# Kernel optimization log

Measured on AMD Instinct MI355X. Metric: run time of the kernel, lower is better.

Reference implementation:

```python
import jax, jax.numpy as jnp
import numpy as np

N_NODES = 100_000
N_EDGES = 800_000
D_EDGE = 64
D_NODE = 64
D_GLOBAL = 64
D_IN = D_EDGE + 2 * D_NODE + D_GLOBAL  # 256
D_HID = 128
D_OUT = 64


def setup_inputs() -> dict:
    key = jax.random.key(0)
    ks = jax.random.split(key, 8)
    edge_feats = jax.random.normal(ks[0], (N_EDGES, D_EDGE), dtype=jnp.float32)
    node_feats = jax.random.normal(ks[1], (N_NODES, D_NODE), dtype=jnp.float32)
    global_attr = jax.random.normal(ks[2], (D_GLOBAL,), dtype=jnp.float32)
    senders = jax.random.randint(ks[3], (N_EDGES,), 0, N_NODES, dtype=jnp.int32)
    receivers = jax.random.randint(ks[4], (N_EDGES,), 0, N_NODES, dtype=jnp.int32)
    W1 = jax.random.normal(ks[5], (D_IN, D_HID), dtype=jnp.float32) * (1.0 / np.sqrt(D_IN))
    b1 = jnp.zeros((D_HID,), dtype=jnp.float32)
    W2 = jax.random.normal(ks[6], (D_HID, D_OUT), dtype=jnp.float32) * (1.0 / np.sqrt(D_HID))
    b2 = jnp.zeros((D_OUT,), dtype=jnp.float32)
    return {
        "edge_feats": edge_feats,
        "node_feats": node_feats,
        "global_attr": global_attr,
        "senders": senders,
        "receivers": receivers,
        "W1": W1, "b1": b1, "W2": W2, "b2": b2,
    }


def reference(edge_feats, node_feats, global_attr, senders, receivers, W1, b1, W2, b2):
    # Per-edge concat of [edge.data, receiver.data, sender.data, global.data]
    # (torch.cat order in the original), stacked over all edges.
    E = edge_feats.shape[0]
    recv = node_feats[receivers]          # [E, D_NODE] gather
    send = node_feats[senders]            # [E, D_NODE] gather
    g = jnp.broadcast_to(global_attr[None, :], (E, global_attr.shape[0]))
    x = jnp.concatenate([edge_feats, recv, send, g], axis=-1)  # [E, 256]
    # Updater MLP on the stacked edge batch.
    h = jax.nn.relu(x @ W1 + b1)          # [E, 128]
    out = h @ W2 + b2                     # [E, 64]
    return out
```

## Files before the change

### kernel.cpp

```cpp
#include <hip/hip_runtime.h>
#include <hip/hip_bf16.h>


typedef __bf16 bf16x8 __attribute__((ext_vector_type(8)));
typedef __bf16 bf16x2 __attribute__((ext_vector_type(2)));
typedef float f32x4 __attribute__((ext_vector_type(4)));

#define GRID_MAIN 2048
#define SWZ(x) ((x) ^ (((x) >> 3) & 7))
#define WS_NODEBF_OFF 66560

__global__ void prep_kernel(const float* __restrict__ W1, const float* __restrict__ b1,
                            const float* __restrict__ W2, const float* __restrict__ gattr,
                            __bf16* __restrict__ W1F, __bf16* __restrict__ W2F,
                            float* __restrict__ g1) {
    int tid = blockIdx.x * blockDim.x + threadIdx.x;
    if (tid < 128 * 192) {
        int n = tid / 192, k = tid % 192;
        int w = n >> 5, nt2 = (n >> 4) & 1, c = n & 15;
        int f = k >> 5, g = (k >> 3) & 3, j = k & 7;
        W1F[((((w * 2 + nt2) * 6 + f) * 64) + c + 16 * g) * 8 + j] = (__bf16)W1[k * 128 + n];
    } else if (tid < 128 * 192 + 64 * 128) {
        int t = tid - 128 * 192;
        int n = t / 128, p = t % 128;
        int w = n >> 4, c = n & 15;
        int ks = p >> 5, g = (p >> 3) & 3, j = p & 7;
        int klog = (p >> 5) * 32 + (p & 1) * 16 + ((p >> 1) & 15);
        W2F[(((w * 4 + ks) * 64) + c + 16 * g) * 8 + j] = (__bf16)W2[klog * 64 + n];
    } else if (tid < 128 * 192 + 64 * 128 + 128) {
        int n = tid - (128 * 192 + 64 * 128);
        float acc = b1[n];
        for (int j = 0; j < 64; ++j) acc += gattr[j] * W1[(192 + j) * 128 + n];
        g1[n] = acc;
    }
}

__global__ __launch_bounds__(256) void node_conv_kernel(const float* __restrict__ nf,
                                                        __bf16* __restrict__ nb, int n8) {
    int t = blockIdx.x * blockDim.x + threadIdx.x;
    if (t < n8) {
        f32x4 a = *(const f32x4*)(nf + (long)t * 8);
        f32x4 b = *(const f32x4*)(nf + (long)t * 8 + 4);
        bf16x8 o;
#pragma unroll
        for (int j = 0; j < 4; ++j) { o[j] = (__bf16)a[j]; o[4 + j] = (__bf16)b[j]; }
        *(bf16x8*)(nb + (long)t * 8) = o;
    }
}

__device__ __forceinline__ f32x4 mk4(float v) {
    f32x4 r; r[0] = v; r[1] = v; r[2] = v; r[3] = v; return r;
}

__device__ __forceinline__ bf16x8 cvt8(f32x4 lo, f32x4 hi) {
    bf16x8 t;
#pragma unroll
    for (int j = 0; j < 4; ++j) { t[j] = (__bf16)lo[j]; t[4 + j] = (__bf16)hi[j]; }
    return t;
}

__global__ __launch_bounds__(256) void edge_mlp_kernel(
    const float* __restrict__ edge_feats, const __bf16* __restrict__ node_bf,
    const int* __restrict__ senders, const int* __restrict__ receivers,
    const __bf16* __restrict__ W1F, const __bf16* __restrict__ W2F,
    const float* __restrict__ g1, const float* __restrict__ b2,
    float* __restrict__ out, int E, int numTiles)
{
    __shared__ __bf16 smem[20480];

    const int lane = threadIdx.x & 63;
    const int w    = threadIdx.x >> 6;
    const int c    = lane & 15;
    const int g    = lane >> 4;
    const int G    = gridDim.x;

    bf16x8 wb1[2][6];
#pragma unroll
    for (int nt2 = 0; nt2 < 2; ++nt2)
#pragma unroll
        for (int f = 0; f < 6; ++f)
            wb1[nt2][f] = *(const bf16x8*)(W1F + (((w * 2 + nt2) * 6 + f) * 64 + lane) * 8);
    bf16x8 wb2[4];
#pragma unroll
    for (int ks = 0; ks < 4; ++ks)
        wb2[ks] = *(const bf16x8*)(W2F + ((w * 4 + ks) * 64 + lane) * 8);
    const float g1v0 = g1[w * 32 + c];
    const float g1v1 = g1[w * 32 + 16 + c];
    const float b2v  = b2[w * 16 + c];

    const int sr = SWZ(c * 4 + g);

    auto rowof = [&](int i) {
        long r_ = ((long)blockIdx.x + (long)i * G) * 64 + w * 16 + c;
        return r_ > (long)E - 1 ? (long)E - 1 : r_;
    };

    bf16x8 snr0, snr1, sns0, sns1;
    f32x4 se0, se1, se2, se3;
    int iRa, iSa, iRb, iSb;
    {
        long r0 = rowof(0);
        int iR0 = receivers[r0], iS0 = senders[r0];
        const __bf16* pr = node_bf + ((long)iR0 << 6) + g * 8;
        const __bf16* ps = node_bf + ((long)iS0 << 6) + g * 8;
        snr0 = *(const bf16x8*)(pr);
        snr1 = *(const bf16x8*)(pr + 32);
        sns0 = *(const bf16x8*)(ps);
        sns1 = *(const bf16x8*)(ps + 32);
        const float* pe = edge_feats + (r0 << 6) + g * 8;
        se0 = *(const f32x4*)(pe);      se1 = *(const f32x4*)(pe + 4);
        se2 = *(const f32x4*)(pe + 32); se3 = *(const f32x4*)(pe + 36);
        long r1 = rowof(1);
        iRa = receivers[r1]; iSa = senders[r1];
        long r2 = rowof(2);
        iRb = receivers[r2]; iSb = senders[r2];
    }

    for (int t = blockIdx.x; t < numTiles; t += G) {
        __bf16* ab = smem + w * 3072 + lane * 8;
        *(bf16x8*)(ab)        = cvt8(se0, se1);
        *(bf16x8*)(ab + 512)  = cvt8(se2, se3);
        *(bf16x8*)(ab + 1024) = snr0;
        *(bf16x8*)(ab + 1536) = snr1;
        *(bf16x8*)(ab + 2048) = sns0;
        *(bf16x8*)(ab + 2560) = sns1;

        {
            const __bf16* pr = node_bf + ((long)iRa << 6) + g * 8;
            const __bf16* ps = node_bf + ((long)iSa << 6) + g * 8;
            snr0 = *(const bf16x8*)(pr);
            snr1 = *(const bf16x8*)(pr + 32);
            sns0 = *(const bf16x8*)(ps);
            sns1 = *(const bf16x8*)(ps + 32);
            long rce = rowof(1);
            rce = ((long)t + G) * 64 + w * 16 + c;
            if (rce > (long)E - 1) rce = (long)E - 1;
            const float* pe = edge_feats + (rce << 6) + g * 8;
            se0 = *(const f32x4*)(pe);      se1 = *(const f32x4*)(pe + 4);
            se2 = *(const f32x4*)(pe + 32); se3 = *(const f32x4*)(pe + 36);
            iRa = iRb; iSa = iSb;
            long r3 = ((long)t + 3L * G) * 64 + w * 16 + c;
            if (r3 > (long)E - 1) r3 = (long)E - 1;
            iRb = receivers[r3]; iSb = senders[r3];
        }
        __builtin_amdgcn_sched_barrier(0);

        asm volatile("s_waitcnt lgkmcnt(0)" ::: "memory");
        __builtin_amdgcn_s_barrier();

        f32x4 acc0[4], acc1[4];
#pragma unroll
        for (int mt = 0; mt < 4; ++mt) { acc0[mt] = mk4(g1v0); acc1[mt] = mk4(g1v1); }
#pragma unroll
        for (int mt = 0; mt < 4; ++mt)
#pragma unroll
            for (int f = 0; f < 6; ++f) {
                bf16x8 a = *(const bf16x8*)(smem + ((mt * 6 + f) * 64 + lane) * 8);
                acc0[mt] = __builtin_amdgcn_mfma_f32_16x16x32_bf16(a, wb1[0][f], acc0[mt], 0, 0, 0);
                acc1[mt] = __builtin_amdgcn_mfma_f32_16x16x32_bf16(a, wb1[1][f], acc1[mt], 0, 0, 0);
            }

#pragma unroll
        for (int mt = 0; mt < 4; ++mt)
#pragma unroll
            for (int r = 0; r < 4; ++r) {
                float v0 = acc0[mt][r]; v0 = v0 > 0.f ? v0 : 0.f;
                float v1 = acc1[mt][r]; v1 = v1 > 0.f ? v1 : 0.f;
                bf16x2 pk; pk[0] = (__bf16)v0; pk[1] = (__bf16)v1;
                int s = g * 16 + r * 4 + (c >> 2);
                s = SWZ(s);
                *(bf16x2*)&smem[12288 + (mt * 4 + w) * 512 + s * 8 + ((c & 3) << 1)] = pk;
            }

        asm volatile("s_waitcnt lgkmcnt(0)" ::: "memory");
        __builtin_amdgcn_s_barrier();

        f32x4 acc2[4];
#pragma unroll
        for (int mt = 0; mt < 4; ++mt) acc2[mt] = mk4(b2v);
#pragma unroll
        for (int mt = 0; mt < 4; ++mt)
#pragma unroll
            for (int ks = 0; ks < 4; ++ks) {
                bf16x8 ah = *(const bf16x8*)&smem[12288 + (mt * 4 + ks) * 512 + sr * 8];
                acc2[mt] = __builtin_amdgcn_mfma_f32_16x16x32_bf16(ah, wb2[ks], acc2[mt], 0, 0, 0);
            }

#pragma unroll
        for (int mt = 0; mt < 4; ++mt)
#pragma unroll
            for (int r = 0; r < 4; ++r) {
                long orow = (long)t * 64 + mt * 16 + g * 4 + r;
                if (orow < E) out[orow * 64 + w * 16 + c] = acc2[mt][r];
            }
    }
}

__global__ __launch_bounds__(256) void edge_mlp_fallback(
    const float* __restrict__ edge_feats, const float* __restrict__ node_feats,
    const int* __restrict__ senders, const int* __restrict__ receivers,
    const __bf16* __restrict__ W1F, const __bf16* __restrict__ W2F,
    const float* __restrict__ g1, const float* __restrict__ b2,
    float* __restrict__ out, int E, int numTiles)
{
    __shared__ __bf16 A_lds[4 * 6 * 64 * 8];
    __shared__ __bf16 h_frag[4 * 4 * 64 * 8];
    const int lane = threadIdx.x & 63;
    const int w = threadIdx.x >> 6;
    const int c = lane & 15;
    const int g = lane >> 4;
    const int G = gridDim.x;

    bf16x8 wb1[2][6];
#pragma unroll
    for (int nt2 = 0; nt2 < 2; ++nt2)
#pragma unroll
        for (int f = 0; f < 6; ++f)
            wb1[nt2][f] = *(const bf16x8*)(W1F + (((w * 2 + nt2) * 6 + f) * 64 + lane) * 8);
    bf16x8 wb2[4];
#pragma unroll
    for (int ks = 0; ks < 4; ++ks)
        wb2[ks] = *(const bf16x8*)(W2F + ((w * 4 + ks) * 64 + lane) * 8);
    const float g1v0 = g1[w * 32 + c];
    const float g1v1 = g1[w * 32 + 16 + c];
    const float b2v  = b2[w * 16 + c];

    for (int t = blockIdx.x; t < numTiles; t += G) {
        long rowc = (long)t * 64 + w * 16 + c;
        if (rowc > (long)E - 1) rowc = (long)E - 1;
        int iR = receivers[rowc], iS = senders[rowc];
        const float* pr = node_feats + ((long)iR << 6) + g * 8;
        const float* ps = node_feats + ((long)iS << 6) + g * 8;
        const float* pe = edge_feats + (rowc << 6) + g * 8;
        f32x4 e0a = *(const f32x4*)(pe),      e0b = *(const f32x4*)(pe + 4);
        f32x4 e1a = *(const f32x4*)(pe + 32), e1b = *(const f32x4*)(pe + 36);
        f32x4 r0a = *(const f32x4*)(pr),      r0b = *(const f32x4*)(pr + 4);
        f32x4 r1a = *(const f32x4*)(pr + 32), r1b = *(const f32x4*)(pr + 36);
        f32x4 s0a = *(const f32x4*)(ps),      s0b = *(const f32x4*)(ps + 4);
        f32x4 s1a = *(const f32x4*)(ps + 32), s1b = *(const f32x4*)(ps + 36);

        __bf16* ab = A_lds + w * 6 * 512 + lane * 8;
        *(bf16x8*)(ab)        = cvt8(e0a, e0b);
        *(bf16x8*)(ab + 512)  = cvt8(e1a, e1b);
        *(bf16x8*)(ab + 1024) = cvt8(r0a, r0b);
        *(bf16x8*)(ab + 1536) = cvt8(r1a, r1b);
        *(bf16x8*)(ab + 2048) = cvt8(s0a, s0b);
        *(bf16x8*)(ab + 2560) = cvt8(s1a, s1b);
        __syncthreads();

        f32x4 acc0[4], acc1[4];
#pragma unroll
        for (int mt = 0; mt < 4; ++mt) { acc0[mt] = mk4(g1v0); acc1[mt] = mk4(g1v1); }
#pragma unroll
        for (int mt = 0; mt < 4; ++mt)
#pragma unroll
            for (int f = 0; f < 6; ++f) {
                bf16x8 a = *(const bf16x8*)(A_lds + ((mt * 6 + f) * 64 + lane) * 8);
                acc0[mt] = __builtin_amdgcn_mfma_f32_16x16x32_bf16(a, wb1[0][f], acc0[mt], 0, 0, 0);
                acc1[mt] = __builtin_amdgcn_mfma_f32_16x16x32_bf16(a, wb1[1][f], acc1[mt], 0, 0, 0);
            }
#pragma unroll
        for (int mt = 0; mt < 4; ++mt)
#pragma unroll
            for (int r = 0; r < 4; ++r) {
                float v0 = acc0[mt][r]; v0 = v0 > 0.f ? v0 : 0.f;
                float v1 = acc1[mt][r]; v1 = v1 > 0.f ? v1 : 0.f;
                bf16x2 pk; pk[0] = (__bf16)v0; pk[1] = (__bf16)v1;
                *(bf16x2*)&h_frag[(((mt * 4 + w) * 64 + (g * 4 + r) * 4 + (c >> 2)) << 3)
                                  + ((c & 3) << 1)] = pk;
            }
        __syncthreads();

        f32x4 acc2[4];
#pragma unroll
        for (int mt = 0; mt < 4; ++mt) acc2[mt] = mk4(b2v);
#pragma unroll
        for (int mt = 0; mt < 4; ++mt)
#pragma unroll
            for (int ks = 0; ks < 4; ++ks) {
                bf16x8 ah = *(const bf16x8*)&h_frag[((mt * 4 + ks) * 64 + c * 4 + g) * 8];
                acc2[mt] = __builtin_amdgcn_mfma_f32_16x16x32_bf16(ah, wb2[ks], acc2[mt], 0, 0, 0);
            }
#pragma unroll
        for (int mt = 0; mt < 4; ++mt)
#pragma unroll
            for (int r = 0; r < 4; ++r) {
                long orow = (long)t * 64 + mt * 16 + g * 4 + r;
                if (orow < E) out[orow * 64 + w * 16 + c] = acc2[mt][r];
            }
        __syncthreads();
    }
}

extern "C" void kernel_launch(void* const* d_in, const int* in_sizes, int n_in,
                              void* d_out, int out_size, void* d_ws, size_t ws_size,
                              hipStream_t stream) {
    const float* edge_feats = (const float*)d_in[0];
    const float* node_feats = (const float*)d_in[1];
    const float* gattr      = (const float*)d_in[2];
    const int*   senders    = (const int*)d_in[3];
    const int*   receivers  = (const int*)d_in[4];
    const float* W1         = (const float*)d_in[5];
    const float* b1         = (const float*)d_in[6];
    const float* W2         = (const float*)d_in[7];
    const float* b2         = (const float*)d_in[8];
    float* out = (float*)d_out;

    const int E = in_sizes[3];
    const int N = in_sizes[1] / 64;

    char* ws = (char*)d_ws;
    __bf16* W1F = (__bf16*)ws;
    __bf16* W2F = (__bf16*)(ws + 49152);
    float*  g1  = (float*)(ws + 49152 + 16384);
    __bf16* nodeBF = (__bf16*)(ws + WS_NODEBF_OFF);

    const size_t ws_needed = (size_t)WS_NODEBF_OFF + (size_t)N * 64 * 2;
    const bool useNB = ws_size >= ws_needed;

    int prep_total = 128 * 192 + 64 * 128 + 128;
    prep_kernel<<<(prep_total + 255) / 256, 256, 0, stream>>>(W1, b1, W2, gattr, W1F, W2F, g1);

    const int numTiles = (E + 63) / 64;
    int grid = numTiles < GRID_MAIN ? numTiles : GRID_MAIN;
    if (useNB) {
        int n8 = N * 8;
        node_conv_kernel<<<(n8 + 255) / 256, 256, 0, stream>>>(node_feats, nodeBF, n8);
        edge_mlp_kernel<<<grid, 256, 0, stream>>>(edge_feats, nodeBF, senders, receivers,
                                                  W1F, W2F, g1, b2, out, E, numTiles);
    } else {
        edge_mlp_fallback<<<grid, 256, 0, stream>>>(edge_feats, node_feats, senders, receivers,
                                                    W1F, W2F, g1, b2, out, E, numTiles);
    }
}
```

Before: 127.6 us.

## Feed first GEMM operands from registers with 16-edge tiles and 2-wave blocks

The main edge kernel now processes 16-edge tiles with 128-thread blocks (two waves). Each wave computes 64 hidden columns directly from register-held A fragments instead of staging the concatenated input through LDS. W1's prepacked layout is permuted for the edge-feature k-slices so contiguous float4 loads map onto MFMA fragments. Only the hidden activations go through a double-buffered LDS buffer, with one barrier per tile instead of two, and the grid doubles to 4096 blocks. This trades larger per-wave weight register footprints (24 W1 fragments) and smaller tiles for fewer LDS round-trips and barriers.

```diff
diff --git a/kernel.cpp b/kernel.cpp
--- a/kernel.cpp
+++ b/kernel.cpp
@@ -6,7 +6,7 @@
 typedef __bf16 bf16x2 __attribute__((ext_vector_type(2)));
 typedef float f32x4 __attribute__((ext_vector_type(4)));
 
-#define GRID_MAIN 2048
+#define GRID_MAIN 4096
 #define SWZ(x) ((x) ^ (((x) >> 3) & 7))
 #define WS_NODEBF_OFF 66560
 
@@ -18,7 +18,15 @@
     if (tid < 128 * 192) {
         int n = tid / 192, k = tid % 192;
         int w = n >> 5, nt2 = (n >> 4) & 1, c = n & 15;
-        int f = k >> 5, g = (k >> 3) & 3, j = k & 7;
+        int f = k >> 5, r = k & 31;
+        int g, j;
+        if (f < 2) {
+            g = (r >> 2) & 3;
+            j = ((r >> 4) & 1) * 4 + (r & 3);
+        } else {
+            g = (r >> 3) & 3;
+            j = r & 7;
+        }
         W1F[((((w * 2 + nt2) * 6 + f) * 64) + c + 16 * g) * 8 + j] = (__bf16)W1[k * 128 + n];
     } else if (tid < 128 * 192 + 64 * 128) {
         int t = tid - 128 * 192;
@@ -59,140 +67,136 @@
     return t;
 }
 
-__global__ __launch_bounds__(256) void edge_mlp_kernel(
+__global__ __launch_bounds__(128, 2) void edge_mlp_kernel(
     const float* __restrict__ edge_feats, const __bf16* __restrict__ node_bf,
     const int* __restrict__ senders, const int* __restrict__ receivers,
     const __bf16* __restrict__ W1F, const __bf16* __restrict__ W2F,
     const float* __restrict__ g1, const float* __restrict__ b2,
     float* __restrict__ out, int E, int numTiles)
 {
-    __shared__ __bf16 smem[20480];
+    __shared__ __bf16 hb[2][2048];
 
     const int lane = threadIdx.x & 63;
-    const int w    = threadIdx.x >> 6;
+    const int v    = threadIdx.x >> 6;
     const int c    = lane & 15;
     const int g    = lane >> 4;
     const int G    = gridDim.x;
 
-    bf16x8 wb1[2][6];
-#pragma unroll
-    for (int nt2 = 0; nt2 < 2; ++nt2)
+    bf16x8 wb1[4][6];
+#pragma unroll
+    for (int nt = 0; nt < 4; ++nt)
 #pragma unroll
         for (int f = 0; f < 6; ++f)
-            wb1[nt2][f] = *(const bf16x8*)(W1F + (((w * 2 + nt2) * 6 + f) * 64 + lane) * 8);
-    bf16x8 wb2[4];
-#pragma unroll
-    for (int ks = 0; ks < 4; ++ks)
-        wb2[ks] = *(const bf16x8*)(W2F + ((w * 4 + ks) * 64 + lane) * 8);
-    const float g1v0 = g1[w * 32 + c];
-    const float g1v1 = g1[w * 32 + 16 + c];
-    const float b2v  = b2[w * 16 + c];
-
+            wb1[nt][f] = *(const bf16x8*)(W1F + (((v * 4 + nt) * 6 + f) * 64 + lane) * 8);
+    bf16x8 wb2[2][4];
+#pragma unroll
+    for (int o = 0; o < 2; ++o)
+#pragma unroll
+        for (int ks = 0; ks < 4; ++ks)
+            wb2[o][ks] = *(const bf16x8*)(W2F + (((v * 2 + o) * 4 + ks) * 64 + lane) * 8);
+    float g1v[4];
+#pragma unroll
+    for (int nt = 0; nt < 4; ++nt) g1v[nt] = g1[v * 64 + nt * 16 + c];
+    float b2v[2];
+#pragma unroll
+    for (int o = 0; o < 2; ++o) b2v[o] = b2[(v * 2 + o) * 16 + c];
     const int sr = SWZ(c * 4 + g);
 
-    auto rowof = [&](int i) {
-        long r_ = ((long)blockIdx.x + (long)i * G) * 64 + w * 16 + c;
-        return r_ > (long)E - 1 ? (long)E - 1 : r_;
-    };
-
-    bf16x8 snr0, snr1, sns0, sns1;
     f32x4 se0, se1, se2, se3;
-    int iRa, iSa, iRb, iSb;
+    bf16x8 sn0, sn1, sn2, sn3;
+    int iRa, iSa;
     {
-        long r0 = rowof(0);
-        int iR0 = receivers[r0], iS0 = senders[r0];
-        const __bf16* pr = node_bf + ((long)iR0 << 6) + g * 8;
-        const __bf16* ps = node_bf + ((long)iS0 << 6) + g * 8;
-        snr0 = *(const bf16x8*)(pr);
-        snr1 = *(const bf16x8*)(pr + 32);
-        sns0 = *(const bf16x8*)(ps);
-        sns1 = *(const bf16x8*)(ps + 32);
-        const float* pe = edge_feats + (r0 << 6) + g * 8;
-        se0 = *(const f32x4*)(pe);      se1 = *(const f32x4*)(pe + 4);
-        se2 = *(const f32x4*)(pe + 32); se3 = *(const f32x4*)(pe + 36);
-        long r1 = rowof(1);
+        long rc = (long)blockIdx.x * 16 + c;
+        if (rc > (long)E - 1) rc = (long)E - 1;
+        int iR = receivers[rc], iS = senders[rc];
+        const __bf16* pr = node_bf + ((long)iR << 6) + g * 8;
+        const __bf16* ps = node_bf + ((long)iS << 6) + g * 8;
+        sn0 = *(const bf16x8*)(pr);
+        sn1 = *(const bf16x8*)(pr + 32);
+        sn2 = *(const bf16x8*)(ps);
+        sn3 = *(const bf16x8*)(ps + 32);
+        const float* pe = edge_feats + (rc << 6) + g * 4;
+        se0 = *(const f32x4*)(pe);
+        se1 = *(const f32x4*)(pe + 16);
+        se2 = *(const f32x4*)(pe + 32);
+        se3 = *(const f32x4*)(pe + 48);
+        long r1 = ((long)blockIdx.x + G) * 16 + c;
+        if (r1 > (long)E - 1) r1 = (long)E - 1;
         iRa = receivers[r1]; iSa = senders[r1];
-        long r2 = rowof(2);
-        iRb = receivers[r2]; iSb = senders[r2];
-    }
-
+    }
+
+    int buf = 0;
     for (int t = blockIdx.x; t < numTiles; t += G) {
-        __bf16* ab = smem + w * 3072 + lane * 8;
-        *(bf16x8*)(ab)        = cvt8(se0, se1);
-        *(bf16x8*)(ab + 512)  = cvt8(se2, se3);
-        *(bf16x8*)(ab + 1024) = snr0;
-        *(bf16x8*)(ab + 1536) = snr1;
-        *(bf16x8*)(ab + 2048) = sns0;
-        *(bf16x8*)(ab + 2560) = sns1;
-
-        {
+        bf16x8 a0 = cvt8(se0, se1);
+        bf16x8 a1 = cvt8(se2, se3);
+        bf16x8 a2 = sn0, a3 = sn1, a4 = sn2, a5 = sn3;
+
+        if (t + G < numTiles) {
             const __bf16* pr = node_bf + ((long)iRa << 6) + g * 8;
             const __bf16* ps = node_bf + ((long)iSa << 6) + g * 8;
-            snr0 = *(const bf16x8*)(pr);
-            snr1 = *(const bf16x8*)(pr + 32);
-            sns0 = *(const bf16x8*)(ps);
-            sns1 = *(const bf16x8*)(ps + 32);
-            long rce = rowof(1);
-            rce = ((long)t + G) * 64 + w * 16 + c;
-            if (rce > (long)E - 1) rce = (long)E - 1;
-            const float* pe = edge_feats + (rce << 6) + g * 8;
-            se0 = *(const f32x4*)(pe);      se1 = *(const f32x4*)(pe + 4);
-            se2 = *(const f32x4*)(pe + 32); se3 = *(const f32x4*)(pe + 36);
-            iRa = iRb; iSa = iSb;
-            long r3 = ((long)t + 3L * G) * 64 + w * 16 + c;
-            if (r3 > (long)E - 1) r3 = (long)E - 1;
-            iRb = receivers[r3]; iSb = senders[r3];
+            sn0 = *(const bf16x8*)(pr);
+            sn1 = *(const bf16x8*)(pr + 32);
+            sn2 = *(const bf16x8*)(ps);
+            sn3 = *(const bf16x8*)(ps + 32);
+            long rn = ((long)t + G) * 16 + c;
+            if (rn > (long)E - 1) rn = (long)E - 1;
+            const float* pe = edge_feats + (rn << 6) + g * 4;
+            se0 = *(const f32x4*)(pe);
+            se1 = *(const f32x4*)(pe + 16);
+            se2 = *(const f32x4*)(pe + 32);
+            se3 = *(const f32x4*)(pe + 48);
+            long r2 = ((long)t + 2L * G) * 16 + c;
+            if (r2 > (long)E - 1) r2 = (long)E - 1;
+            iRa = receivers[r2]; iSa = senders[r2];
         }
         __builtin_amdgcn_sched_barrier(0);
 
+        f32x4 acc[4];
+#pragma unroll
+        for (int nt = 0; nt < 4; ++nt) acc[nt] = mk4(g1v[nt]);
+#pragma unroll
+        for (int nt = 0; nt < 4; ++nt) {
+            acc[nt] = __builtin_amdgcn_mfma_f32_16x16x32_bf16(a0, wb1[nt][0], acc[nt], 0, 0, 0);
+            acc[nt] = __builtin_amdgcn_mfma_f32_16x16x32_bf16(a1, wb1[nt][1], acc[nt], 0, 0, 0);
+            acc[nt] = __builtin_amdgcn_mfma_f32_16x16x32_bf16(a2, wb1[nt][2], acc[nt], 0, 0, 0);
+            acc[nt] = __builtin_amdgcn_mfma_f32_16x16x32_bf16(a3, wb1[nt][3], acc[nt], 0, 0, 0);
+            acc[nt] = __builtin_amdgcn_mfma_f32_16x16x32_bf16(a4, wb1[nt][4], acc[nt], 0, 0, 0);
+            acc[nt] = __builtin_amdgcn_mfma_f32_16x16x32_bf16(a5, wb1[nt][5], acc[nt], 0, 0, 0);
+        }
+
+#pragma unroll
+        for (int np2 = 0; np2 < 2; ++np2)
+#pragma unroll
+            for (int r = 0; r < 4; ++r) {
+                float v0 = acc[np2 * 2][r];     v0 = v0 > 0.f ? v0 : 0.f;
+                float v1 = acc[np2 * 2 + 1][r]; v1 = v1 > 0.f ? v1 : 0.f;
+                bf16x2 pk; pk[0] = (__bf16)v0; pk[1] = (__bf16)v1;
+                int s = SWZ(g * 16 + r * 4 + (c >> 2));
+                *(bf16x2*)&hb[buf][(v * 2 + np2) * 512 + s * 8 + ((c & 3) << 1)] = pk;
+            }
+
         asm volatile("s_waitcnt lgkmcnt(0)" ::: "memory");
         __builtin_amdgcn_s_barrier();
 
-        f32x4 acc0[4], acc1[4];
-#pragma unroll
-        for (int mt = 0; mt < 4; ++mt) { acc0[mt] = mk4(g1v0); acc1[mt] = mk4(g1v1); }
-#pragma unroll
-        for (int mt = 0; mt < 4; ++mt)
-#pragma unroll
-            for (int f = 0; f < 6; ++f) {
-                bf16x8 a = *(const bf16x8*)(smem + ((mt * 6 + f) * 64 + lane) * 8);
-                acc0[mt] = __builtin_amdgcn_mfma_f32_16x16x32_bf16(a, wb1[0][f], acc0[mt], 0, 0, 0);
-                acc1[mt] = __builtin_amdgcn_mfma_f32_16x16x32_bf16(a, wb1[1][f], acc1[mt], 0, 0, 0);
-            }
-
-#pragma unroll
-        for (int mt = 0; mt < 4; ++mt)
+        f32x4 acc2[2];
+#pragma unroll
+        for (int o = 0; o < 2; ++o) acc2[o] = mk4(b2v[o]);
+#pragma unroll
+        for (int ks = 0; ks < 4; ++ks) {
+            bf16x8 ah = *(const bf16x8*)&hb[buf][ks * 512 + sr * 8];
+            acc2[0] = __builtin_amdgcn_mfma_f32_16x16x32_bf16(ah, wb2[0][ks], acc2[0], 0, 0, 0);
+            acc2[1] = __builtin_amdgcn_mfma_f32_16x16x32_bf16(ah, wb2[1][ks], acc2[1], 0, 0, 0);
+        }
+
+#pragma unroll
+        for (int o = 0; o < 2; ++o)
 #pragma unroll
             for (int r = 0; r < 4; ++r) {
-                float v0 = acc0[mt][r]; v0 = v0 > 0.f ? v0 : 0.f;
-                float v1 = acc1[mt][r]; v1 = v1 > 0.f ? v1 : 0.f;
-                bf16x2 pk; pk[0] = (__bf16)v0; pk[1] = (__bf16)v1;
-                int s = g * 16 + r * 4 + (c >> 2);
-                s = SWZ(s);
-                *(bf16x2*)&smem[12288 + (mt * 4 + w) * 512 + s * 8 + ((c & 3) << 1)] = pk;
-            }
-
-        asm volatile("s_waitcnt lgkmcnt(0)" ::: "memory");
-        __builtin_amdgcn_s_barrier();
-
-        f32x4 acc2[4];
-#pragma unroll
-        for (int mt = 0; mt < 4; ++mt) acc2[mt] = mk4(b2v);
-#pragma unroll
-        for (int mt = 0; mt < 4; ++mt)
-#pragma unroll
-            for (int ks = 0; ks < 4; ++ks) {
-                bf16x8 ah = *(const bf16x8*)&smem[12288 + (mt * 4 + ks) * 512 + sr * 8];
-                acc2[mt] = __builtin_amdgcn_mfma_f32_16x16x32_bf16(ah, wb2[ks], acc2[mt], 0, 0, 0);
-            }
-
-#pragma unroll
-        for (int mt = 0; mt < 4; ++mt)
-#pragma unroll
-            for (int r = 0; r < 4; ++r) {
-                long orow = (long)t * 64 + mt * 16 + g * 4 + r;
-                if (orow < E) out[orow * 64 + w * 16 + c] = acc2[mt][r];
-            }
+                long orow = (long)t * 16 + g * 4 + r;
+                if (orow < E) out[orow * 64 + (v * 2 + o) * 16 + c] = acc2[o][r];
+            }
+
+        buf ^= 1;
     }
 }
 
@@ -224,6 +228,7 @@
     const float g1v0 = g1[w * 32 + c];
     const float g1v1 = g1[w * 32 + 16 + c];
     const float b2v  = b2[w * 16 + c];
+    const int sr = SWZ(c * 4 + g);
 
     for (int t = blockIdx.x; t < numTiles; t += G) {
         long rowc = (long)t * 64 + w * 16 + c;
@@ -231,9 +236,9 @@
         int iR = receivers[rowc], iS = senders[rowc];
         const float* pr = node_feats + ((long)iR << 6) + g * 8;
         const float* ps = node_feats + ((long)iS << 6) + g * 8;
-        const float* pe = edge_feats + (rowc << 6) + g * 8;
-        f32x4 e0a = *(const f32x4*)(pe),      e0b = *(const f32x4*)(pe + 4);
-        f32x4 e1a = *(const f32x4*)(pe + 32), e1b = *(const f32x4*)(pe + 36);
+        const float* pe = edge_feats + (rowc << 6) + g * 4;
+        f32x4 e0a = *(const f32x4*)(pe),      e0b = *(const f32x4*)(pe + 16);
+        f32x4 e1a = *(const f32x4*)(pe + 32), e1b = *(const f32x4*)(pe + 48);
         f32x4 r0a = *(const f32x4*)(pr),      r0b = *(const f32x4*)(pr + 4);
         f32x4 r1a = *(const f32x4*)(pr + 32), r1b = *(const f32x4*)(pr + 36);
         f32x4 s0a = *(const f32x4*)(ps),      s0b = *(const f32x4*)(ps + 4);
@@ -266,8 +271,8 @@
                 float v0 = acc0[mt][r]; v0 = v0 > 0.f ? v0 : 0.f;
                 float v1 = acc1[mt][r]; v1 = v1 > 0.f ? v1 : 0.f;
                 bf16x2 pk; pk[0] = (__bf16)v0; pk[1] = (__bf16)v1;
-                *(bf16x2*)&h_frag[(((mt * 4 + w) * 64 + (g * 4 + r) * 4 + (c >> 2)) << 3)
-                                  + ((c & 3) << 1)] = pk;
+                int s = SWZ(g * 16 + r * 4 + (c >> 2));
+                *(bf16x2*)&h_frag[((mt * 4 + w) * 512) + s * 8 + ((c & 3) << 1)] = pk;
             }
         __syncthreads();
 
@@ -278,7 +283,7 @@
         for (int mt = 0; mt < 4; ++mt)
 #pragma unroll
             for (int ks = 0; ks < 4; ++ks) {
-                bf16x8 ah = *(const bf16x8*)&h_frag[((mt * 4 + ks) * 64 + c * 4 + g) * 8];
+                bf16x8 ah = *(const bf16x8*)&h_frag[(mt * 4 + ks) * 512 + sr * 8];
                 acc2[mt] = __builtin_amdgcn_mfma_f32_16x16x32_bf16(ah, wb2[ks], acc2[mt], 0, 0, 0);
             }
 #pragma unroll
@@ -321,15 +326,17 @@
     int prep_total = 128 * 192 + 64 * 128 + 128;
     prep_kernel<<<(prep_total + 255) / 256, 256, 0, stream>>>(W1, b1, W2, gattr, W1F, W2F, g1);
 
-    const int numTiles = (E + 63) / 64;
-    int grid = numTiles < GRID_MAIN ? numTiles : GRID_MAIN;
     if (useNB) {
         int n8 = N * 8;
         node_conv_kernel<<<(n8 + 255) / 256, 256, 0, stream>>>(node_feats, nodeBF, n8);
-        edge_mlp_kernel<<<grid, 256, 0, stream>>>(edge_feats, nodeBF, senders, receivers,
-                                                  W1F, W2F, g1, b2, out, E, numTiles);
+        const int numTiles16 = (E + 15) / 16;
+        int grid = numTiles16 < GRID_MAIN ? numTiles16 : GRID_MAIN;
+        edge_mlp_kernel<<<grid, 128, 0, stream>>>(edge_feats, nodeBF, senders, receivers,
+                                                  W1F, W2F, g1, b2, out, E, numTiles16);
     } else {
+        const int numTiles64 = (E + 63) / 64;
+        int grid = numTiles64 < 2048 ? numTiles64 : 2048;
         edge_mlp_fallback<<<grid, 256, 0, stream>>>(edge_feats, node_feats, senders, receivers,
-                                                    W1F, W2F, g1, b2, out, E, numTiles);
-    }
-}
+                                                    W1F, W2F, g1, b2, out, E, numTiles64);
+    }
+}
```

Result: slower. 166.2 us (+30.3%).
